# Performance work log

Hardware: AMD Instinct MI355X
Metric: run time of the kernel (lower is better)

The kernel has to match this reference:

```python
import jax, jax.numpy as jnp
import numpy as np

K_MAX_X = 16
K_MAX_T = 16


def _k_actual(N, k_max):
    # low-mode indices [0..k_max] ++ [N-k_max..N-1], mapped to signed frequencies
    idx = np.concatenate([np.arange(k_max + 1), np.arange(N - k_max, N)]).astype(np.float32)
    return np.where(idx <= (N - 1) // 2, idx, idx - N)


def _phase(N, k_max, sign):
    # separable 1D truncated DFT factor: exp(sign*2*pi*i*k*n/N)/sqrt(N), shape [modes, N]
    k = _k_actual(N, k_max)
    n = np.arange(N, dtype=np.float32)
    ang = sign * 2.0 * np.pi * k[:, None] * n[None, :] / N
    return jnp.asarray((np.exp(1j * ang) / np.sqrt(N)).astype(np.complex64))


def setup_inputs() -> dict:
    key = jax.random.key(0)
    k1, k2, k3 = jax.random.split(key, 3)
    B, C_in, C_out, H, W = 16, 64, 64, 128, 128
    modes = 2 * K_MAX_X + 1  # 33
    scale = 1.0 / (C_in * C_out)
    x = jax.random.normal(k1, (B, C_in, H, W), dtype=jnp.float32)
    wr = scale * jax.random.uniform(k2, (C_in, C_out, modes, modes), dtype=jnp.float32)
    wi = scale * jax.random.uniform(k3, (C_in, C_out, modes, modes), dtype=jnp.float32)
    return {"x": x, "weights_real": wr, "weights_imag": wi}


def reference(x, weights_real, weights_imag):
    B, C, H, W = x.shape
    Px_f = _phase(H, K_MAX_X, -1.0)  # [mx, H]
    Pt_f = _phase(W, K_MAX_T, -1.0)  # [mt, W]
    Px_i = _phase(H, K_MAX_X, +1.0)
    Pt_i = _phase(W, K_MAX_T, +1.0)
    xc = x.astype(jnp.complex64)
    # truncated 2D DFT (separable): X[b,c,i,j]
    X = jnp.einsum('bcnm,in,jm->bcij', xc, Px_f, Pt_f)
    R = (weights_real + 1j * weights_imag).astype(jnp.complex64)
    out_kept = jnp.einsum('bcij,coij->boij', X, R)
    # truncated inverse DFT back to grid
    out = jnp.einsum('boij,in,jm->bonm', out_kept, Px_i, Pt_i)
    return jnp.real(out)
```

## Files before the change

kernel.cpp:

```cpp
#include <hip/hip_runtime.h>


#define NB   16
#define NC   64
#define NO   64
#define NH   128
#define NW   128
#define NM   33
#define WMODE (NM*NM)
#define MPAD  1092
#define NIMG 1024

typedef __attribute__((ext_vector_type(8))) short s8v;
typedef __attribute__((ext_vector_type(4))) float f4v;

__device__ inline unsigned short f2bf(float f) {
  union { float f; unsigned u; } v; v.f = f;
  unsigned r = (v.u + 0x7FFFu + ((v.u >> 16) & 1u)) >> 16;
  return (unsigned short)r;
}

__device__ inline s8v pack8(float4 a, float4 b) {
  s8v r;
  r[0] = (short)f2bf(a.x); r[1] = (short)f2bf(a.y);
  r[2] = (short)f2bf(a.z); r[3] = (short)f2bf(a.w);
  r[4] = (short)f2bf(b.x); r[5] = (short)f2bf(b.y);
  r[6] = (short)f2bf(b.z); r[7] = (short)f2bf(b.w);
  return r;
}

__device__ inline uint2 pack4(f4v a) {
  uint2 p;
  p.x = (unsigned)f2bf(a[0]) | ((unsigned)f2bf(a[1]) << 16);
  p.y = (unsigned)f2bf(a[2]) | ((unsigned)f2bf(a[3]) << 16);
  return p;
}

__device__ inline unsigned short phase_bf(int f, int x) {
  if (f >= 66) return 0;
  int g = (f < 33) ? f : f - 33;
  int fr = (g <= 16) ? g : g + 95;
  int ph = (fr * x) & 127;
  float ang = (float)ph * 0.04908738521234052f;
  float v = ((f < 33) ? cosf(ang) : sinf(ang)) * 0.08838834764831845f;
  return f2bf(v);
}

__global__ __launch_bounds__(256) void spc_tables(short* __restrict__ T1,
                                                  short* __restrict__ T2,
                                                  short* __restrict__ T3,
                                                  short* __restrict__ T4) {
  int tid = blockIdx.x * 256 + threadIdx.x;
  if (tid >= 49152) return;
  int f, x; short* dst;
  if (tid < 10240) {
    int e = tid & 7, l = (tid >> 3) & 63, q = tid >> 9;
    int ks = q / 5, jt = q - 5 * ks;
    f = jt * 16 + (l & 15); x = ks * 32 + (l >> 4) * 8 + e; dst = T1 + tid;
  } else if (tid < 20480) {
    int u = tid - 10240;
    int e = u & 7, l = (u >> 3) & 63, q = u >> 9;
    int it = q >> 2, ks = q & 3;
    f = it * 16 + (l & 15); x = ks * 32 + (l >> 4) * 8 + e; dst = T2 + u;
  } else if (tid < 36864) {
    int u = tid - 20480;
    int e = u & 7, l = (u >> 3) & 63, q = u >> 9;
    int cs = q >> 4, ks = (q >> 3) & 1, mt = q & 7;
    int j = ks * 32 + (l >> 4) * 8 + e;
    f = (j < 33) ? cs * 33 + j : 66;
    x = mt * 16 + (l & 15); dst = T3 + u;
  } else {
    int u = tid - 36864;
    int e = u & 7, l = (u >> 3) & 63, q = u >> 9;
    int nt = q / 3, ks = q - 3 * nt;
    int i2 = ks * 32 + (l >> 4) * 8 + e;
    if (i2 < 48) f = (i2 < 33) ? i2 : 66;
    else         f = (i2 - 48 < 33) ? 33 + (i2 - 48) : 66;
    x = nt * 16 + (l & 15); dst = T4 + u;
  }
  *dst = (short)phase_bf(f, x);
}

__global__ __launch_bounds__(256) void spc_fwd_mfma(const float* __restrict__ x,
                                                    const s8v* __restrict__ T1,
                                                    const s8v* __restrict__ T2,
                                                    unsigned* __restrict__ X2u) {
  __shared__ short Wt[80 * 128];
  __shared__ float Gs[80 * 84];
  const int t = threadIdx.x;
  const int l = t & 63;
  const int w = t >> 6;
  const int lr = l & 15;
  const int lg = l >> 4;
  const int img = blockIdx.x;
  const float* xp = x + (size_t)img * (NH * NW);

  for (int nn = 0; nn < 2; ++nn) {
    const int nt = 2 * w + nn;
    const float* xrow = xp + (nt * 16 + lr) * NW + lg * 8;
    s8v a[4];
#pragma unroll
    for (int ks = 0; ks < 4; ++ks) {
      float4 f0 = *reinterpret_cast<const float4*>(xrow + ks * 32);
      float4 f1 = *reinterpret_cast<const float4*>(xrow + ks * 32 + 4);
      a[ks] = pack8(f0, f1);
    }
#pragma unroll
    for (int jt = 0; jt < 5; ++jt) {
      f4v acc = {0.f, 0.f, 0.f, 0.f};
#pragma unroll
      for (int ks = 0; ks < 4; ++ks) {
        s8v b = T1[(ks * 5 + jt) * 64 + l];
        acc = __builtin_amdgcn_mfma_f32_16x16x32_bf16(a[ks], b, acc, 0, 0, 0);
      }
      int j = jt * 16 + lr;
      int g = ((nt * 16 + lg * 4) >> 2) ^ ((j & 7) << 2);
      *reinterpret_cast<uint2*>(&Wt[j * 128 + g * 4]) = pack4(acc);
    }
  }
  __syncthreads();

  for (int tix = w; tix < 25; tix += 4) {
    int it = tix / 5, j2 = tix - 5 * it;
    int jrow = j2 * 16 + lr;
    f4v acc = {0.f, 0.f, 0.f, 0.f};
#pragma unroll
    for (int ks = 0; ks < 4; ++ks) {
      s8v afr = T2[(it * 4 + ks) * 64 + l];
      int g = (ks * 8 + lg * 2) ^ ((jrow & 7) << 2);
      s8v b = *reinterpret_cast<const s8v*>(&Wt[jrow * 128 + g * 4]);
      acc = __builtin_amdgcn_mfma_f32_16x16x32_bf16(afr, b, acc, 0, 0, 0);
    }
    int gi = it * 16 + lg * 4;
#pragma unroll
    for (int r = 0; r < 4; ++r) Gs[(gi + r) * 84 + jrow] = acc[r];
  }
  __syncthreads();

  unsigned* X2p = X2u + (size_t)img * WMODE;
  for (int idx = t; idx < WMODE; idx += 256) {
    int i = idx / 33, j = idx - 33 * i;
    float g11 = Gs[i * 84 + j];
    float g22 = Gs[(i + 33) * 84 + (j + 33)];
    float g12 = Gs[i * 84 + (j + 33)];
    float g21 = Gs[(i + 33) * 84 + j];
    X2p[idx] = (unsigned)f2bf(g11 - g22) | ((unsigned)f2bf(-(g12 + g21)) << 16);
  }
}

__global__ __launch_bounds__(512) void spc_vmix(const float* __restrict__ wr,
                                                const float* __restrict__ wi,
                                                const unsigned* __restrict__ X2u,
                                                short* __restrict__ Kbf) {
  const int t = threadIdx.x;
  const int ml = t & 63;
  const int w = t >> 6;
  const int b0 = w * 2;
  const int o0 = blockIdx.x * 2;
  const int m0 = blockIdx.y * 64;
  const int m = m0 + ml;
  const int mc = (m > 1088) ? 1088 : m;

  const float* wrp = wr + (size_t)o0 * WMODE + mc;
  const float* wip = wi + (size_t)o0 * WMODE + mc;
  const unsigned* xp = X2u + (size_t)(b0 * 64) * WMODE + mc;
  const size_t cstepW = (size_t)64 * WMODE;

  float aR[2][2], aI[2][2];
#pragma unroll
  for (int j = 0; j < 2; ++j)
#pragma unroll
    for (int oo = 0; oo < 2; ++oo) { aR[j][oo] = 0.f; aI[j][oo] = 0.f; }

#pragma unroll 1
  for (int c4 = 0; c4 < 16; ++c4) {
    float wrv[4][2], wiv[4][2];
    unsigned u[4][2];
#pragma unroll
    for (int q = 0; q < 4; ++q) {
      const int c = c4 * 4 + q;
#pragma unroll
      for (int oo = 0; oo < 2; ++oo) {
        wrv[q][oo] = wrp[(size_t)c * cstepW + (size_t)oo * WMODE];
        wiv[q][oo] = wip[(size_t)c * cstepW + (size_t)oo * WMODE];
      }
#pragma unroll
      for (int j = 0; j < 2; ++j)
        u[q][j] = xp[(size_t)(j * 64 + c) * WMODE];
    }
#pragma unroll
    for (int q = 0; q < 4; ++q) {
#pragma unroll
      for (int j = 0; j < 2; ++j) {
        union { unsigned uu; float f; } cv;
        cv.uu = u[q][j] << 16;         const float xr_ = cv.f;
        cv.uu = u[q][j] & 0xFFFF0000u; const float xi_ = cv.f;
#pragma unroll
        for (int oo = 0; oo < 2; ++oo) {
          aR[j][oo] = fmaf(xr_, wrv[q][oo], fmaf(-xi_, wiv[q][oo], aR[j][oo]));
          aI[j][oo] = fmaf(xr_, wiv[q][oo], fmaf( xi_, wrv[q][oo], aI[j][oo]));
        }
      }
    }
  }

  if (m < WMODE) {
#pragma unroll
    for (int j = 0; j < 2; ++j)
#pragma unroll
      for (int oo = 0; oo < 2; ++oo) {
        size_t img = (size_t)(b0 + j) * 64 + o0 + oo;
        Kbf[img * (2 * MPAD) + m]        = (short)f2bf(aR[j][oo]);
        Kbf[img * (2 * MPAD) + MPAD + m] = (short)f2bf(aI[j][oo]);
      }
  }
}

__global__ __launch_bounds__(256) void spc_inv_mfma(const short* __restrict__ Kbf,
                                                    const s8v* __restrict__ T3,
                                                    const s8v* __restrict__ T4,
                                                    float* __restrict__ out) {
  __shared__ short Kls2[2 * MPAD];
  __shared__ short Vt[128 * 128];
  const int t = threadIdx.x;
  const int l = t & 63;
  const int w = t >> 6;
  const int lr = l & 15;
  const int lg = l >> 4;
  const int img = blockIdx.x;

  {
    const uint4* src = reinterpret_cast<const uint4*>(Kbf + (size_t)img * (2 * MPAD));
    uint4* dstl = reinterpret_cast<uint4*>(Kls2);
    for (int idx = t; idx < 273; idx += 256) dstl[idx] = src[idx];
  }
  __syncthreads();

  s8v fr[2][3][2];
#pragma unroll
  for (int ri2 = 0; ri2 < 2; ++ri2)
#pragma unroll
    for (int it = 0; it < 3; ++it)
#pragma unroll
      for (int ks = 0; ks < 2; ++ks) {
        const int i = it * 16 + lr;
#pragma unroll
        for (int e = 0; e < 8; ++e) {
          const int j = ks * 32 + lg * 8 + e;
          unsigned short v = (i < 33 && j < 33)
              ? (unsigned short)Kls2[ri2 * MPAD + i * 33 + j] : (unsigned short)0;
          fr[ri2][it][ks][e] = (short)v;
        }
      }

  for (int mm = 0; mm < 2; ++mm) {
    const int mt = w * 2 + mm;
    const int m = mt * 16 + lr;
    s8v cw[2], sw[2], nsw[2];
#pragma unroll
    for (int ks = 0; ks < 2; ++ks) {
      cw[ks] = T3[((0 * 2 + ks) * 8 + mt) * 64 + l];
      sw[ks] = T3[((1 * 2 + ks) * 8 + mt) * 64 + l];
#pragma unroll
      for (int e = 0; e < 8; ++e)
        nsw[ks][e] = (short)(((unsigned short)sw[ks][e]) ^ 0x8000u);
    }
#pragma unroll
    for (int it = 0; it < 3; ++it) {
      f4v t1 = {0.f, 0.f, 0.f, 0.f}, t2 = {0.f, 0.f, 0.f, 0.f};
#pragma unroll
      for (int ks = 0; ks < 2; ++ks) {
        t1 = __builtin_amdgcn_mfma_f32_16x16x32_bf16(fr[0][it][ks], cw[ks],  t1, 0, 0, 0);
        t1 = __builtin_amdgcn_mfma_f32_16x16x32_bf16(fr[1][it][ks], nsw[ks], t1, 0, 0, 0);
        t2 = __builtin_amdgcn_mfma_f32_16x16x32_bf16(fr[1][it][ks], cw[ks],  t2, 0, 0, 0);
        t2 = __builtin_amdgcn_mfma_f32_16x16x32_bf16(fr[0][it][ks], sw[ks],  t2, 0, 0, 0);
      }
      const int base1 = it * 16 + lg * 4;
      const int g1 = (base1 >> 2) ^ ((m & 7) << 2);
      *reinterpret_cast<uint2*>(&Vt[m * 128 + g1 * 4]) = pack4(t1);
      f4v nt2v = {-t2[0], -t2[1], -t2[2], -t2[3]};
      const int g2 = ((48 + base1) >> 2) ^ ((m & 7) << 2);
      *reinterpret_cast<uint2*>(&Vt[m * 128 + g2 * 4]) = pack4(nt2v);
    }
  }
  __syncthreads();

  float* op = out + (size_t)img * (NH * NW);
  for (int nn = 0; nn < 2; ++nn) {
    const int nt = w * 2 + nn;
    s8v a[3];
#pragma unroll
    for (int ks = 0; ks < 3; ++ks) a[ks] = T4[(nt * 3 + ks) * 64 + l];
    for (int mt = 0; mt < 8; ++mt) {
      const int m = mt * 16 + lr;
      f4v acc = {0.f, 0.f, 0.f, 0.f};
#pragma unroll
      for (int ks = 0; ks < 3; ++ks) {
        const int g = (ks * 8 + lg * 2) ^ ((m & 7) << 2);
        s8v bb = *reinterpret_cast<const s8v*>(&Vt[m * 128 + g * 4]);
        acc = __builtin_amdgcn_mfma_f32_16x16x32_bf16(a[ks], bb, acc, 0, 0, 0);
      }
      const int n = nt * 16 + lg * 4;
#pragma unroll
      for (int r = 0; r < 4; ++r) op[(n + r) * NW + m] = acc[r];
    }
  }
}

extern "C" void kernel_launch(void* const* d_in, const int* in_sizes, int n_in,
                              void* d_out, int out_size, void* d_ws, size_t ws_size,
                              hipStream_t stream) {
  const float* x  = (const float*)d_in[0];
  const float* wr = (const float*)d_in[1];
  const float* wi = (const float*)d_in[2];
  float* out = (float*)d_out;

  char* ws = (char*)d_ws;
  short* T1 = (short*)(ws);
  short* T2 = (short*)(ws + 20480);
  short* T3 = (short*)(ws + 40960);
  short* T4 = (short*)(ws + 73728);
  unsigned* X2u = (unsigned*)(ws + 98304);
  short* Kbf = (short*)(ws + 4558848);

  hipLaunchKernelGGL(spc_tables, dim3(192), dim3(256), 0, stream, T1, T2, T3, T4);
  hipLaunchKernelGGL(spc_fwd_mfma, dim3(NIMG), dim3(256), 0, stream,
                     x, (const s8v*)T1, (const s8v*)T2, X2u);
  hipLaunchKernelGGL(spc_vmix, dim3(32, 18), dim3(512), 0, stream,
                     wr, wi, X2u, Kbf);
  hipLaunchKernelGGL(spc_inv_mfma, dim3(NIMG), dim3(256), 0, stream,
                     Kbf, (const s8v*)T3, (const s8v*)T4, out);
}
```

Measured before the change: 76.56 us.

## Prepack spectral weights to bf16 tiled layout and stage them in LDS

Adds a pre-pass kernel that converts the fp32 real and imaginary weights into packed bf16 pairs, reordered into per-(output-pair, mode-chunk) tiles. The mixing kernel then copies its tile into shared memory once per block, so its eight warps no longer each re-read the weights from global memory. This aims to cut redundant cache traffic and halve the bytes the mixing kernel reads. In exchange it adds a full extra read and write pass over the weights on every call, and lowers weight precision to bf16.

```diff
diff --git a/kernel.cpp b/kernel.cpp
--- a/kernel.cpp
+++ b/kernel.cpp
@@ -10,6 +10,8 @@
 #define WMODE (NM*NM)
 #define MPAD  1092
 #define NIMG 1024
+#define NTOT (64*64*WMODE)
+#define CPLANE (64*WMODE)
 
 typedef __attribute__((ext_vector_type(8))) short s8v;
 typedef __attribute__((ext_vector_type(4))) float f4v;
@@ -18,6 +20,13 @@
   union { float f; unsigned u; } v; v.f = f;
   unsigned r = (v.u + 0x7FFFu + ((v.u >> 16) & 1u)) >> 16;
   return (unsigned short)r;
+}
+
+__device__ inline float bflo(unsigned u) {
+  union { unsigned u; float f; } cv; cv.u = u << 16; return cv.f;
+}
+__device__ inline float bfhi(unsigned u) {
+  union { unsigned u; float f; } cv; cv.u = u & 0xFFFF0000u; return cv.f;
 }
 
 __device__ inline s8v pack8(float4 a, float4 b) {
@@ -81,6 +90,49 @@
   *dst = (short)phase_bf(f, x);
 }
 
+__global__ __launch_bounds__(256) void spc_wpack(const float* __restrict__ wr,
+                                                 const float* __restrict__ wi,
+                                                 unsigned* __restrict__ Wpk) {
+  const int t = threadIdx.x;
+  const size_t base = (size_t)blockIdx.x * 8192;
+#pragma unroll 1
+  for (int p = 0; p < 8; ++p) {
+    const size_t L = base + (size_t)p * 1024 + (size_t)t * 4;
+    if (L + 4 <= (size_t)NTOT) {
+      float4 a = *reinterpret_cast<const float4*>(wr + L);
+      float4 b = *reinterpret_cast<const float4*>(wi + L);
+      float ae[4] = {a.x, a.y, a.z, a.w};
+      float be[4] = {b.x, b.y, b.z, b.w};
+#pragma unroll
+      for (int e = 0; e < 4; ++e) {
+        unsigned Li = (unsigned)L + e;
+        unsigned c = Li / (unsigned)CPLANE;
+        unsigned rem = Li - c * (unsigned)CPLANE;
+        unsigned o = rem / (unsigned)WMODE;
+        unsigned m = rem - o * (unsigned)WMODE;
+        unsigned mch = m >> 6, ml = m & 63u;
+        size_t D = ((((size_t)(o >> 1) * 18 + mch) * 64 + c) * 2 + (o & 1)) * 64 + ml;
+        Wpk[D] = (unsigned)f2bf(ae[e]) | ((unsigned)f2bf(be[e]) << 16);
+      }
+    } else {
+#pragma unroll
+      for (int e = 0; e < 4; ++e) {
+        size_t Li = L + e;
+        if (Li < (size_t)NTOT) {
+          unsigned Lu = (unsigned)Li;
+          unsigned c = Lu / (unsigned)CPLANE;
+          unsigned rem = Lu - c * (unsigned)CPLANE;
+          unsigned o = rem / (unsigned)WMODE;
+          unsigned m = rem - o * (unsigned)WMODE;
+          unsigned mch = m >> 6, ml = m & 63u;
+          size_t D = ((((size_t)(o >> 1) * 18 + mch) * 64 + c) * 2 + (o & 1)) * 64 + ml;
+          Wpk[D] = (unsigned)f2bf(wr[Li]) | ((unsigned)f2bf(wi[Li]) << 16);
+        }
+      }
+    }
+  }
+}
+
 __global__ __launch_bounds__(256) void spc_fwd_mfma(const float* __restrict__ x,
                                                     const s8v* __restrict__ T1,
                                                     const s8v* __restrict__ T2,
@@ -148,23 +200,30 @@
   }
 }
 
-__global__ __launch_bounds__(512) void spc_vmix(const float* __restrict__ wr,
-                                                const float* __restrict__ wi,
+__global__ __launch_bounds__(512) void spc_vmix(const unsigned* __restrict__ Wpk,
                                                 const unsigned* __restrict__ X2u,
                                                 short* __restrict__ Kbf) {
+  __shared__ unsigned Ls[8192];
   const int t = threadIdx.x;
   const int ml = t & 63;
   const int w = t >> 6;
   const int b0 = w * 2;
-  const int o0 = blockIdx.x * 2;
-  const int m0 = blockIdx.y * 64;
-  const int m = m0 + ml;
+  const int opair = blockIdx.x;
+  const int mch = blockIdx.y;
+  const int o0 = opair * 2;
+  const int m = mch * 64 + ml;
   const int mc = (m > 1088) ? 1088 : m;
 
-  const float* wrp = wr + (size_t)o0 * WMODE + mc;
-  const float* wip = wi + (size_t)o0 * WMODE + mc;
+  {
+    const uint4* src = reinterpret_cast<const uint4*>(
+        Wpk + ((size_t)opair * 18 + mch) * 8192);
+    uint4* dst = reinterpret_cast<uint4*>(Ls);
+#pragma unroll
+    for (int p = 0; p < 4; ++p) dst[p * 512 + t] = src[p * 512 + t];
+  }
+  __syncthreads();
+
   const unsigned* xp = X2u + (size_t)(b0 * 64) * WMODE + mc;
-  const size_t cstepW = (size_t)64 * WMODE;
 
   float aR[2][2], aI[2][2];
 #pragma unroll
@@ -174,32 +233,29 @@
 
 #pragma unroll 1
   for (int c4 = 0; c4 < 16; ++c4) {
-    float wrv[4][2], wiv[4][2];
     unsigned u[4][2];
 #pragma unroll
     for (int q = 0; q < 4; ++q) {
       const int c = c4 * 4 + q;
 #pragma unroll
-      for (int oo = 0; oo < 2; ++oo) {
-        wrv[q][oo] = wrp[(size_t)c * cstepW + (size_t)oo * WMODE];
-        wiv[q][oo] = wip[(size_t)c * cstepW + (size_t)oo * WMODE];
-      }
-#pragma unroll
       for (int j = 0; j < 2; ++j)
         u[q][j] = xp[(size_t)(j * 64 + c) * WMODE];
     }
 #pragma unroll
     for (int q = 0; q < 4; ++q) {
+      const int c = c4 * 4 + q;
+      const unsigned w0 = Ls[(c * 2 + 0) * 64 + ml];
+      const unsigned w1 = Ls[(c * 2 + 1) * 64 + ml];
+      const float wr0 = bflo(w0), wi0 = bfhi(w0);
+      const float wr1 = bflo(w1), wi1 = bfhi(w1);
 #pragma unroll
       for (int j = 0; j < 2; ++j) {
-        union { unsigned uu; float f; } cv;
-        cv.uu = u[q][j] << 16;         const float xr_ = cv.f;
-        cv.uu = u[q][j] & 0xFFFF0000u; const float xi_ = cv.f;
-#pragma unroll
-        for (int oo = 0; oo < 2; ++oo) {
-          aR[j][oo] = fmaf(xr_, wrv[q][oo], fmaf(-xi_, wiv[q][oo], aR[j][oo]));
-          aI[j][oo] = fmaf(xr_, wiv[q][oo], fmaf( xi_, wrv[q][oo], aI[j][oo]));
-        }
+        const float xr_ = bflo(u[q][j]);
+        const float xi_ = bfhi(u[q][j]);
+        aR[j][0] = fmaf(xr_, wr0, fmaf(-xi_, wi0, aR[j][0]));
+        aI[j][0] = fmaf(xr_, wi0, fmaf( xi_, wr0, aI[j][0]));
+        aR[j][1] = fmaf(xr_, wr1, fmaf(-xi_, wi1, aR[j][1]));
+        aI[j][1] = fmaf(xr_, wi1, fmaf( xi_, wr1, aI[j][1]));
       }
     }
   }
@@ -322,12 +378,14 @@
   short* T4 = (short*)(ws + 73728);
   unsigned* X2u = (unsigned*)(ws + 98304);
   short* Kbf = (short*)(ws + 4558848);
+  unsigned* Wpk = (unsigned*)(ws + 9031680);
 
   hipLaunchKernelGGL(spc_tables, dim3(192), dim3(256), 0, stream, T1, T2, T3, T4);
+  hipLaunchKernelGGL(spc_wpack, dim3(545), dim3(256), 0, stream, wr, wi, Wpk);
   hipLaunchKernelGGL(spc_fwd_mfma, dim3(NIMG), dim3(256), 0, stream,
                      x, (const s8v*)T1, (const s8v*)T2, X2u);
   hipLaunchKernelGGL(spc_vmix, dim3(32, 18), dim3(512), 0, stream,
-                     wr, wi, X2u, Kbf);
+                     Wpk, X2u, Kbf);
   hipLaunchKernelGGL(spc_inv_mfma, dim3(NIMG), dim3(256), 0, stream,
                      Kbf, (const s8v*)T3, (const s8v*)T4, out);
 }
```

New measurement: 76.06 us. No clear change (-0.7%).
